# Kernel optimization log

Hardware: AMD Instinct MI355X
Metric: run time of the kernel (lower is better)

The kernel has to match this reference:

```python
import jax, jax.numpy as jnp
import numpy as np

B, N, D_IN, D_OUT = 8, 2048, 1024, 1024


def setup_inputs() -> dict:
    key = jax.random.key(0)
    k0, k1, k2, k3 = jax.random.split(key, 4)
    scale = 1.0 / np.sqrt(D_IN)
    x = jax.random.normal(k0, (B, N, D_IN), dtype=jnp.float32)
    Wq = jax.random.normal(k1, (D_IN, D_OUT), dtype=jnp.float32) * scale
    Wk = jax.random.normal(k2, (D_IN, D_OUT), dtype=jnp.float32) * scale
    Wv = jax.random.normal(k3, (D_IN, D_OUT), dtype=jnp.float32) * scale
    return {"x": x, "Wq": Wq, "Wk": Wk, "Wv": Wv}


def reference(x, Wq, Wk, Wv):
    # x: [b, n, d_in]; single-head causal attention, dropout p=0 (eval).
    q = jnp.einsum('bnd,de->bne', x, Wq)
    k = jnp.einsum('bnd,de->bne', x, Wk)
    v = jnp.einsum('bnd,de->bne', x, Wv)
    n = x.shape[1]
    scores = jnp.einsum('bqe,bke->bqk', q, k)  # [b, n, n]
    causal_mask = jnp.triu(jnp.ones((n, n), dtype=bool), k=1)
    scores = jnp.where(causal_mask, -jnp.inf, scores)
    scale = 1.0 / jnp.sqrt(jnp.asarray(k.shape[-1], dtype=scores.dtype))
    attn = jax.nn.softmax(scores * scale, axis=-1)
    context = jnp.einsum('bqk,bke->bqe', attn, v)
    return context
```

## Files before the change

### kernel.cpp

```cpp
#include <hip/hip_runtime.h>


typedef unsigned short u16;
typedef __bf16 bf16x8 __attribute__((ext_vector_type(8)));
typedef float f32x4 __attribute__((ext_vector_type(4)));
typedef unsigned short u16x8 __attribute__((ext_vector_type(8)));
typedef unsigned short u16x4 __attribute__((ext_vector_type(4)));

static constexpr int BATCH = 8;
static constexpr int SEQ = 2048;
static constexpr int DIM = 1024;

static constexpr size_t SZ_XB = (size_t)BATCH * SEQ * DIM * 2;
static constexpr size_t SZ_W  = (size_t)DIM * DIM * 2;
static constexpr size_t OFF_XB  = 0;
static constexpr size_t OFF_WQT = OFF_XB + SZ_XB;
static constexpr size_t OFF_WKT = OFF_WQT + SZ_W;
static constexpr size_t OFF_WVT = OFF_WKT + SZ_W;
static constexpr size_t OFF_Q   = OFF_WVT + SZ_W;
static constexpr size_t OFF_K   = OFF_Q + SZ_XB;
static constexpr size_t OFF_VT  = OFF_K + SZ_XB;
static constexpr size_t OFF_E   = OFF_VT + SZ_XB;
static constexpr size_t OFF_RS  = OFF_E + (size_t)BATCH * SEQ * SEQ * 2;

__device__ __forceinline__ u16 f2b(float f) {
  unsigned u = __builtin_bit_cast(unsigned, f);
  u += 0x7fffu + ((u >> 16) & 1u);
  return (u16)(u >> 16);
}

__device__ __forceinline__ float b2f(u16 b) {
  return __builtin_bit_cast(float, ((unsigned)b) << 16);
}

__device__ __forceinline__ void gload16(const u16* g, u16* l) {
  __builtin_amdgcn_global_load_lds((__attribute__((address_space(1))) void*)g,
                                   (__attribute__((address_space(3))) void*)l, 16, 0, 0);
}

#define VWAIT(N) asm volatile("s_waitcnt vmcnt(" #N ")" ::: "memory")

__device__ __forceinline__ void barrier_raw() {
  __builtin_amdgcn_sched_barrier(0);
  __builtin_amdgcn_s_barrier();
  __builtin_amdgcn_sched_barrier(0);
}

__global__ __launch_bounds__(256) void cast_f32_bf16(const float* __restrict__ in,
                                                     u16* __restrict__ out) {
  const size_t i = ((size_t)blockIdx.x * 256 + threadIdx.x) * 8;
  float4 a = *(const float4*)(in + i);
  float4 b = *(const float4*)(in + i + 4);
  u16x8 o;
  o[0] = f2b(a.x); o[1] = f2b(a.y); o[2] = f2b(a.z); o[3] = f2b(a.w);
  o[4] = f2b(b.x); o[5] = f2b(b.y); o[6] = f2b(b.z); o[7] = f2b(b.w);
  *reinterpret_cast<u16x8*>(out + i) = o;
}

__global__ __launch_bounds__(256) void transpose_cast_w(const float* __restrict__ W,
                                                        u16* __restrict__ WT) {
  __shared__ float t[32][33];
  const int k0 = blockIdx.x * 32, n0 = blockIdx.y * 32;
  const int tx = threadIdx.x, ty = threadIdx.y;
#pragma unroll
  for (int dy = 0; dy < 32; dy += 8)
    t[ty + dy][tx] = W[(size_t)(k0 + ty + dy) * DIM + n0 + tx];
  __syncthreads();
#pragma unroll
  for (int dy = 0; dy < 32; dy += 8)
    WT[(size_t)(n0 + ty + dy) * DIM + k0 + tx] = f2b(t[tx][ty + dy]);
}

template <int MODE>
__global__ __launch_bounds__(512, 4) void gemm128(
    const u16* __restrict__ A, size_t sA, int lda,
    const u16* __restrict__ Bt, size_t sB, int ldb,
    void* __restrict__ C, size_t sC, int ldc,
    int Kdim, float scale,
    void* __restrict__ C2, void* __restrict__ C3, float* __restrict__ rs) {
  const int bx = blockIdx.x, bz = blockIdx.z;
  int by = (int)blockIdx.y;
  if (MODE == 3) by = (bz < 4) ? (15 - by) : by;
  if (MODE == 2 && 2 * bx > by) return;
  const u16* Ab = A + (size_t)bz * sA;
  const u16* Bb = Bt + (size_t)bz * sB;
  const int rowTile = by * 128, colTile = bx * 256;
  int kmax = Kdim;
  if (MODE == 3) {
    int km = (by + 1) * 128;
    if (km < kmax) kmax = km;
  }
  const int NT = kmax >> 5;

  __shared__ __align__(16) u16 lds[3 * 12288];

  const int tid = threadIdx.x;
  const int w = tid >> 6, l = tid & 63;
  const int wm = w >> 2, wn = w & 3;
  const int lr = l & 15, quad = l >> 4;

  auto srow = [](int c) { int u = (c & 7) ^ ((c >> 3) & 7); return 2 * (c >> 3) + (u >> 2); };
  auto skq  = [](int c) { int u = (c & 7) ^ ((c >> 3) & 7); return u & 3; };
  const u16* pA0 = Ab + (size_t)(rowTile + srow(tid)) * lda + skq(tid) * 8;
  const u16* pB0 = Bb + (size_t)(colTile + srow(tid)) * ldb + skq(tid) * 8;
  const u16* pB1 = Bb + (size_t)(colTile + srow(tid + 512)) * ldb + skq(tid + 512) * 8;

  int offA[4], offB[4];
#pragma unroll
  for (int mi = 0; mi < 4; ++mi) {
    const int row = wm * 64 + mi * 16 + lr;
    offA[mi] = ((row * 64 + quad * 16) ^ (((row >> 1) & 7) << 4)) >> 1;
  }
#pragma unroll
  for (int ni = 0; ni < 4; ++ni) {
    const int row = wn * 64 + ni * 16 + lr;
    offB[ni] = 4096 + ((((row * 64 + quad * 16) ^ (((row >> 1) & 7) << 4))) >> 1);
  }

  f32x4 acc[4][4];
#pragma unroll
  for (int i = 0; i < 4; ++i)
#pragma unroll
    for (int j = 0; j < 4; ++j) acc[i][j] = (f32x4){0.f, 0.f, 0.f, 0.f};

#define STAGE(tt)                                   \
  {                                                 \
    u16* sb = &lds[((unsigned)(tt) % 3u) * 12288];  \
    const int ko = (tt) * 32;                       \
    gload16(pA0 + ko, sb + w * 512);                \
    gload16(pB0 + ko, sb + 4096 + w * 512);         \
    gload16(pB1 + ko, sb + 8192 + w * 512);         \
  }

  STAGE(0);
  STAGE(1);
  VWAIT(3);
  barrier_raw();

  for (int t = 0; t < NT; ++t) {
    const u16* S = &lds[((unsigned)t % 3u) * 12288];
    bf16x8 af[4], bf[4];
#pragma unroll
    for (int mi = 0; mi < 4; ++mi)
      af[mi] = *reinterpret_cast<const bf16x8*>(&S[offA[mi]]);
#pragma unroll
    for (int ni = 0; ni < 4; ++ni)
      bf[ni] = *reinterpret_cast<const bf16x8*>(&S[offB[ni]]);
    if (t + 2 < NT) STAGE(t + 2);
    __builtin_amdgcn_s_setprio(1);
#pragma unroll
    for (int mi = 0; mi < 4; ++mi)
#pragma unroll
      for (int ni = 0; ni < 4; ++ni)
        acc[mi][ni] =
            __builtin_amdgcn_mfma_f32_16x16x32_bf16(af[mi], bf[ni], acc[mi][ni], 0, 0, 0);
    __builtin_amdgcn_s_setprio(0);
    if (t + 2 < NT) {
      VWAIT(3);
    } else if (t + 1 < NT) {
      VWAIT(0);
    }
    asm volatile("s_waitcnt lgkmcnt(0)" ::: "memory");
    barrier_raw();
  }
#undef STAGE

  const int orow0 = rowTile + wm * 64 + quad * 4;
  const int ocol0 = colTile + wn * 64 + lr;

  if (MODE == 4) {
    const int which = colTile >> 10;
    if (which < 2) {
      u16* dst = (which == 0) ? (u16*)C : (u16*)C2;
      const int colL0 = ocol0 & 1023;
#pragma unroll
      for (int mi = 0; mi < 4; ++mi)
#pragma unroll
        for (int ni = 0; ni < 4; ++ni) {
          const int colg = colL0 + ni * 16;
#pragma unroll
          for (int r = 0; r < 4; ++r) {
            const int rowg = orow0 + mi * 16 + r;
            dst[(size_t)rowg * DIM + colg] = f2b(acc[mi][ni][r]);
          }
        }
    } else {
      u16* dst = (u16*)C3;
      const int colL0 = ocol0 & 1023;
#pragma unroll
      for (int mi = 0; mi < 4; ++mi) {
        const int rowg0 = orow0 + mi * 16;
        const int bb = rowg0 >> 11, nn = rowg0 & (SEQ - 1);
#pragma unroll
        for (int ni = 0; ni < 4; ++ni) {
          const int colg = colL0 + ni * 16;
          u16x4 pk;
#pragma unroll
          for (int r = 0; r < 4; ++r) pk[r] = f2b(acc[mi][ni][r]);
          *reinterpret_cast<u16x4*>(
              &dst[(size_t)bb * ((size_t)DIM * SEQ) + (size_t)colg * SEQ + nn]) = pk;
        }
      }
    }
  } else if (MODE == 2) {
#pragma unroll
    for (int mi = 0; mi < 4; ++mi) {
      float rloc[4] = {0.f, 0.f, 0.f, 0.f};
#pragma unroll
      for (int ni = 0; ni < 4; ++ni) {
        const int colg = ocol0 + ni * 16;
#pragma unroll
        for (int r = 0; r < 4; ++r) {
          const int rowg = orow0 + mi * 16 + r;
          const float e = (colg <= rowg) ? __expf(acc[mi][ni][r] * scale) : 0.f;
          const u16 pk = f2b(e);
          ((u16*)C)[(size_t)bz * sC + (size_t)rowg * ldc + colg] = pk;
          rloc[r] += b2f(pk);
        }
      }
#pragma unroll
      for (int r = 0; r < 4; ++r) {
        float v = rloc[r];
        v += __shfl_xor(v, 1);
        v += __shfl_xor(v, 2);
        v += __shfl_xor(v, 4);
        v += __shfl_xor(v, 8);
        if (lr == 0) atomicAdd(&rs[bz * SEQ + orow0 + mi * 16 + r], v);
      }
    }
  } else {
#pragma unroll
    for (int mi = 0; mi < 4; ++mi) {
      float linv[4];
#pragma unroll
      for (int r = 0; r < 4; ++r) linv[r] = 1.f / rs[bz * SEQ + orow0 + mi * 16 + r];
#pragma unroll
      for (int ni = 0; ni < 4; ++ni) {
        const int colg = ocol0 + ni * 16;
#pragma unroll
        for (int r = 0; r < 4; ++r) {
          const int rowg = orow0 + mi * 16 + r;
          ((float*)C)[(size_t)bz * sC + (size_t)rowg * ldc + colg] =
              acc[mi][ni][r] * linv[r];
        }
      }
    }
  }
}

extern "C" void kernel_launch(void* const* d_in, const int* in_sizes, int n_in,
                              void* d_out, int out_size, void* d_ws, size_t ws_size,
                              hipStream_t stream) {
  const float* x = (const float*)d_in[0];
  const float* Wq = (const float*)d_in[1];
  const float* Wk = (const float*)d_in[2];
  const float* Wv = (const float*)d_in[3];
  float* out = (float*)d_out;
  char* ws = (char*)d_ws;

  u16* xb = (u16*)(ws + OFF_XB);
  u16* wqT = (u16*)(ws + OFF_WQT);
  u16* wkT = (u16*)(ws + OFF_WKT);
  u16* wvT = (u16*)(ws + OFF_WVT);
  u16* qb = (u16*)(ws + OFF_Q);
  u16* kb = (u16*)(ws + OFF_K);
  u16* vt = (u16*)(ws + OFF_VT);
  u16* eb = (u16*)(ws + OFF_E);
  float* rsum = (float*)(ws + OFF_RS);

  const int total = BATCH * SEQ * DIM;
  cast_f32_bf16<<<total / (256 * 8), 256, 0, stream>>>(x, xb);
  transpose_cast_w<<<dim3(32, 32), dim3(32, 8), 0, stream>>>(Wq, wqT);
  transpose_cast_w<<<dim3(32, 32), dim3(32, 8), 0, stream>>>(Wk, wkT);
  transpose_cast_w<<<dim3(32, 32), dim3(32, 8), 0, stream>>>(Wv, wvT);
  hipMemsetAsync(rsum, 0, (size_t)BATCH * SEQ * sizeof(float), stream);

  gemm128<4><<<dim3(12, 128, 1), 512, 0, stream>>>(
      xb, 0, DIM, wqT, 0, DIM, qb, 0, DIM, DIM, 1.f, kb, vt, nullptr);
  gemm128<2><<<dim3(8, 16, BATCH), 512, 0, stream>>>(
      qb, (size_t)SEQ * DIM, DIM, kb, (size_t)SEQ * DIM, DIM, eb, (size_t)SEQ * SEQ, SEQ,
      DIM, 0.03125f, nullptr, nullptr, rsum);
  gemm128<3><<<dim3(4, 16, BATCH), 512, 0, stream>>>(
      eb, (size_t)SEQ * SEQ, SEQ, vt, (size_t)DIM * SEQ, SEQ, out, (size_t)SEQ * DIM, DIM,
      SEQ, 1.f, nullptr, nullptr, rsum);
}
```

Measured before the change: 365.4 us.

## Remap GEMM grids to 1D with XCD swizzle, compact causal tiles, pair PV rows

All three GEMMs now use a 1D grid whose block index is remapped with an (o&7)-based swizzle, so that neighbouring tiles land on the same XCD. The QK^T launch enumerates only the causal lower-triangle tiles instead of launching and early-exiting the masked ones. The PV kernel gives each block two row tiles (15-by and by) so every block does the same total K-length of work. The three weight transposes are merged into one launch, and the row-sum memset moves into the projection kernel. This cuts launch overhead, idle blocks and load imbalance, but it relies on the projection kernel having finished zeroing the row sums before the QK^T kernel runs.

Result: no change. 363.0 us (-0.7%).

```diff
diff --git a/kernel.cpp b/kernel.cpp
--- a/kernel.cpp
+++ b/kernel.cpp
@@ -15,9 +15,7 @@
 static constexpr size_t SZ_W  = (size_t)DIM * DIM * 2;
 static constexpr size_t OFF_XB  = 0;
 static constexpr size_t OFF_WQT = OFF_XB + SZ_XB;
-static constexpr size_t OFF_WKT = OFF_WQT + SZ_W;
-static constexpr size_t OFF_WVT = OFF_WKT + SZ_W;
-static constexpr size_t OFF_Q   = OFF_WVT + SZ_W;
+static constexpr size_t OFF_Q   = OFF_WQT + 3 * SZ_W;
 static constexpr size_t OFF_K   = OFF_Q + SZ_XB;
 static constexpr size_t OFF_VT  = OFF_K + SZ_XB;
 static constexpr size_t OFF_E   = OFF_VT + SZ_XB;
@@ -57,9 +55,13 @@
   *reinterpret_cast<u16x8*>(out + i) = o;
 }
 
-__global__ __launch_bounds__(256) void transpose_cast_w(const float* __restrict__ W,
-                                                        u16* __restrict__ WT) {
+__global__ __launch_bounds__(256) void transpose_cast_w3(const float* __restrict__ W0,
+                                                         const float* __restrict__ W1,
+                                                         const float* __restrict__ W2,
+                                                         u16* __restrict__ WT) {
   __shared__ float t[32][33];
+  const float* W = (blockIdx.z == 0) ? W0 : (blockIdx.z == 1) ? W1 : W2;
+  u16* dst = WT + (size_t)blockIdx.z * DIM * DIM;
   const int k0 = blockIdx.x * 32, n0 = blockIdx.y * 32;
   const int tx = threadIdx.x, ty = threadIdx.y;
 #pragma unroll
@@ -68,7 +70,7 @@
   __syncthreads();
 #pragma unroll
   for (int dy = 0; dy < 32; dy += 8)
-    WT[(size_t)(n0 + ty + dy) * DIM + k0 + tx] = f2b(t[tx][ty + dy]);
+    dst[(size_t)(n0 + ty + dy) * DIM + k0 + tx] = f2b(t[tx][ty + dy]);
 }
 
 template <int MODE>
@@ -78,31 +80,48 @@
     void* __restrict__ C, size_t sC, int ldc,
     int Kdim, float scale,
     void* __restrict__ C2, void* __restrict__ C3, float* __restrict__ rs) {
-  const int bx = blockIdx.x, bz = blockIdx.z;
-  int by = (int)blockIdx.y;
-  if (MODE == 3) by = (bz < 4) ? (15 - by) : by;
-  if (MODE == 2 && 2 * bx > by) return;
+  const int tid = threadIdx.x;
+
+  int bx = 0, by = 0, bz = 0, by0 = 0;
+  if (MODE == 4) {
+    if (blockIdx.x == 0) {
+      for (int i = tid; i < BATCH * SEQ; i += 512) rs[i] = 0.f;
+    }
+    const int o = (int)blockIdx.x;
+    const int nw = (o & 7) * 192 + (o >> 3);
+    bx = nw % 12; by = nw / 12;
+  } else if (MODE == 2) {
+    const int o = (int)blockIdx.x;
+    const int nw = (o & 7) * 72 + (o >> 3);
+    bz = nw / 72;
+    int i = nw % 72;
+    int cum = 0;
+#pragma unroll
+    for (int y = 0; y < 16; ++y) {
+      const int c = (y >> 1) + 1;
+      if (i < cum + c) { by = y; bx = i - cum; break; }
+      cum += c;
+    }
+  } else {
+    const int o = (int)blockIdx.x;
+    const int nw = (o & 7) * 32 + (o >> 3);
+    bz = nw >> 5; by0 = (nw >> 2) & 7; bx = nw & 3;
+  }
+
   const u16* Ab = A + (size_t)bz * sA;
   const u16* Bb = Bt + (size_t)bz * sB;
-  const int rowTile = by * 128, colTile = bx * 256;
-  int kmax = Kdim;
-  if (MODE == 3) {
-    int km = (by + 1) * 128;
-    if (km < kmax) kmax = km;
-  }
-  const int NT = kmax >> 5;
+  const int colTile = bx * 256;
 
   __shared__ __align__(16) u16 lds[3 * 12288];
 
-  const int tid = threadIdx.x;
   const int w = tid >> 6, l = tid & 63;
   const int wm = w >> 2, wn = w & 3;
   const int lr = l & 15, quad = l >> 4;
 
   auto srow = [](int c) { int u = (c & 7) ^ ((c >> 3) & 7); return 2 * (c >> 3) + (u >> 2); };
   auto skq  = [](int c) { int u = (c & 7) ^ ((c >> 3) & 7); return u & 3; };
-  const u16* pA0 = Ab + (size_t)(rowTile + srow(tid)) * lda + skq(tid) * 8;
-  const u16* pB0 = Bb + (size_t)(colTile + srow(tid)) * ldb + skq(tid) * 8;
+  const int srA = srow(tid), skA = skq(tid);
+  const u16* pB0 = Bb + (size_t)(colTile + srA) * ldb + skA * 8;
   const u16* pB1 = Bb + (size_t)(colTile + srow(tid + 512)) * ldb + skq(tid + 512) * 8;
 
   int offA[4], offB[4];
@@ -116,12 +135,6 @@
     const int row = wn * 64 + ni * 16 + lr;
     offB[ni] = 4096 + ((((row * 64 + quad * 16) ^ (((row >> 1) & 7) << 4))) >> 1);
   }
-
-  f32x4 acc[4][4];
-#pragma unroll
-  for (int i = 0; i < 4; ++i)
-#pragma unroll
-    for (int j = 0; j < 4; ++j) acc[i][j] = (f32x4){0.f, 0.f, 0.f, 0.f};
 
 #define STAGE(tt)                                   \
   {                                                 \
@@ -132,120 +145,136 @@
     gload16(pB1 + ko, sb + 8192 + w * 512);         \
   }
 
-  STAGE(0);
-  STAGE(1);
-  VWAIT(3);
-  barrier_raw();
-
-  for (int t = 0; t < NT; ++t) {
-    const u16* S = &lds[((unsigned)t % 3u) * 12288];
-    bf16x8 af[4], bf[4];
-#pragma unroll
-    for (int mi = 0; mi < 4; ++mi)
-      af[mi] = *reinterpret_cast<const bf16x8*>(&S[offA[mi]]);
-#pragma unroll
-    for (int ni = 0; ni < 4; ++ni)
-      bf[ni] = *reinterpret_cast<const bf16x8*>(&S[offB[ni]]);
-    if (t + 2 < NT) STAGE(t + 2);
-    __builtin_amdgcn_s_setprio(1);
-#pragma unroll
-    for (int mi = 0; mi < 4; ++mi)
+  const int npass = (MODE == 3) ? 2 : 1;
+  for (int pass = 0; pass < npass; ++pass) {
+    const int byp = (MODE == 3) ? (pass == 0 ? 15 - by0 : by0) : by;
+    const int rowTile = byp * 128;
+    int kmax = Kdim;
+    if (MODE == 3) kmax = (byp + 1) * 128;
+    const int NT = kmax >> 5;
+
+    const u16* pA0 = Ab + (size_t)(rowTile + srA) * lda + skA * 8;
+
+    f32x4 acc[4][4];
+#pragma unroll
+    for (int i = 0; i < 4; ++i)
+#pragma unroll
+      for (int j = 0; j < 4; ++j) acc[i][j] = (f32x4){0.f, 0.f, 0.f, 0.f};
+
+    STAGE(0);
+    STAGE(1);
+    VWAIT(3);
+    barrier_raw();
+
+    for (int t = 0; t < NT; ++t) {
+      const u16* S = &lds[((unsigned)t % 3u) * 12288];
+      bf16x8 af[4], bf[4];
+#pragma unroll
+      for (int mi = 0; mi < 4; ++mi)
+        af[mi] = *reinterpret_cast<const bf16x8*>(&S[offA[mi]]);
 #pragma unroll
       for (int ni = 0; ni < 4; ++ni)
-        acc[mi][ni] =
-            __builtin_amdgcn_mfma_f32_16x16x32_bf16(af[mi], bf[ni], acc[mi][ni], 0, 0, 0);
-    __builtin_amdgcn_s_setprio(0);
-    if (t + 2 < NT) {
-      VWAIT(3);
-    } else if (t + 1 < NT) {
-      VWAIT(0);
+        bf[ni] = *reinterpret_cast<const bf16x8*>(&S[offB[ni]]);
+      if (t + 2 < NT) STAGE(t + 2);
+      __builtin_amdgcn_s_setprio(1);
+#pragma unroll
+      for (int mi = 0; mi < 4; ++mi)
+#pragma unroll
+        for (int ni = 0; ni < 4; ++ni)
+          acc[mi][ni] =
+              __builtin_amdgcn_mfma_f32_16x16x32_bf16(af[mi], bf[ni], acc[mi][ni], 0, 0, 0);
+      __builtin_amdgcn_s_setprio(0);
+      if (t + 2 < NT) {
+        VWAIT(3);
+      } else if (t + 1 < NT) {
+        VWAIT(0);
+      }
+      asm volatile("s_waitcnt lgkmcnt(0)" ::: "memory");
+      barrier_raw();
     }
-    asm volatile("s_waitcnt lgkmcnt(0)" ::: "memory");
-    barrier_raw();
-  }
-#undef STAGE
-
-  const int orow0 = rowTile + wm * 64 + quad * 4;
-  const int ocol0 = colTile + wn * 64 + lr;
-
-  if (MODE == 4) {
-    const int which = colTile >> 10;
-    if (which < 2) {
-      u16* dst = (which == 0) ? (u16*)C : (u16*)C2;
+
+    const int orow0 = rowTile + wm * 64 + quad * 4;
+    const int ocol0 = colTile + wn * 64 + lr;
+
+    if (MODE == 4) {
+      const int which = colTile >> 10;
       const int colL0 = ocol0 & 1023;
-#pragma unroll
-      for (int mi = 0; mi < 4; ++mi)
+      if (which < 2) {
+        u16* dst = (which == 0) ? (u16*)C : (u16*)C2;
+#pragma unroll
+        for (int mi = 0; mi < 4; ++mi)
+#pragma unroll
+          for (int ni = 0; ni < 4; ++ni) {
+            const int colg = colL0 + ni * 16;
+#pragma unroll
+            for (int r = 0; r < 4; ++r) {
+              const int rowg = orow0 + mi * 16 + r;
+              dst[(size_t)rowg * DIM + colg] = f2b(acc[mi][ni][r]);
+            }
+          }
+      } else {
+        u16* dst = (u16*)C3;
+#pragma unroll
+        for (int mi = 0; mi < 4; ++mi) {
+          const int rowg0 = orow0 + mi * 16;
+          const int bb = rowg0 >> 11, nn = rowg0 & (SEQ - 1);
+#pragma unroll
+          for (int ni = 0; ni < 4; ++ni) {
+            const int colg = colL0 + ni * 16;
+            u16x4 pk;
+#pragma unroll
+            for (int r = 0; r < 4; ++r) pk[r] = f2b(acc[mi][ni][r]);
+            *reinterpret_cast<u16x4*>(
+                &dst[(size_t)bb * ((size_t)DIM * SEQ) + (size_t)colg * SEQ + nn]) = pk;
+          }
+        }
+      }
+    } else if (MODE == 2) {
+#pragma unroll
+      for (int mi = 0; mi < 4; ++mi) {
+        float rloc[4] = {0.f, 0.f, 0.f, 0.f};
 #pragma unroll
         for (int ni = 0; ni < 4; ++ni) {
-          const int colg = colL0 + ni * 16;
+          const int colg = ocol0 + ni * 16;
 #pragma unroll
           for (int r = 0; r < 4; ++r) {
             const int rowg = orow0 + mi * 16 + r;
-            dst[(size_t)rowg * DIM + colg] = f2b(acc[mi][ni][r]);
+            const float e = (colg <= rowg) ? __expf(acc[mi][ni][r] * scale) : 0.f;
+            const u16 pk = f2b(e);
+            ((u16*)C)[(size_t)bz * sC + (size_t)rowg * ldc + colg] = pk;
+            rloc[r] += b2f(pk);
           }
         }
+#pragma unroll
+        for (int r = 0; r < 4; ++r) {
+          float v = rloc[r];
+          v += __shfl_xor(v, 1);
+          v += __shfl_xor(v, 2);
+          v += __shfl_xor(v, 4);
+          v += __shfl_xor(v, 8);
+          if (lr == 0) atomicAdd(&rs[bz * SEQ + orow0 + mi * 16 + r], v);
+        }
+      }
     } else {
-      u16* dst = (u16*)C3;
-      const int colL0 = ocol0 & 1023;
 #pragma unroll
       for (int mi = 0; mi < 4; ++mi) {
-        const int rowg0 = orow0 + mi * 16;
-        const int bb = rowg0 >> 11, nn = rowg0 & (SEQ - 1);
+        float linv[4];
+#pragma unroll
+        for (int r = 0; r < 4; ++r) linv[r] = 1.f / rs[bz * SEQ + orow0 + mi * 16 + r];
 #pragma unroll
         for (int ni = 0; ni < 4; ++ni) {
-          const int colg = colL0 + ni * 16;
-          u16x4 pk;
-#pragma unroll
-          for (int r = 0; r < 4; ++r) pk[r] = f2b(acc[mi][ni][r]);
-          *reinterpret_cast<u16x4*>(
-              &dst[(size_t)bb * ((size_t)DIM * SEQ) + (size_t)colg * SEQ + nn]) = pk;
+          const int colg = ocol0 + ni * 16;
+#pragma unroll
+          for (int r = 0; r < 4; ++r) {
+            const int rowg = orow0 + mi * 16 + r;
+            ((float*)C)[(size_t)bz * sC + (size_t)rowg * ldc + colg] =
+                acc[mi][ni][r] * linv[r];
+          }
         }
       }
     }
-  } else if (MODE == 2) {
-#pragma unroll
-    for (int mi = 0; mi < 4; ++mi) {
-      float rloc[4] = {0.f, 0.f, 0.f, 0.f};
-#pragma unroll
-      for (int ni = 0; ni < 4; ++ni) {
-        const int colg = ocol0 + ni * 16;
-#pragma unroll
-        for (int r = 0; r < 4; ++r) {
-          const int rowg = orow0 + mi * 16 + r;
-          const float e = (colg <= rowg) ? __expf(acc[mi][ni][r] * scale) : 0.f;
-          const u16 pk = f2b(e);
-          ((u16*)C)[(size_t)bz * sC + (size_t)rowg * ldc + colg] = pk;
-          rloc[r] += b2f(pk);
-        }
-      }
-#pragma unroll
-      for (int r = 0; r < 4; ++r) {
-        float v = rloc[r];
-        v += __shfl_xor(v, 1);
-        v += __shfl_xor(v, 2);
-        v += __shfl_xor(v, 4);
-        v += __shfl_xor(v, 8);
-        if (lr == 0) atomicAdd(&rs[bz * SEQ + orow0 + mi * 16 + r], v);
-      }
-    }
-  } else {
-#pragma unroll
-    for (int mi = 0; mi < 4; ++mi) {
-      float linv[4];
-#pragma unroll
-      for (int r = 0; r < 4; ++r) linv[r] = 1.f / rs[bz * SEQ + orow0 + mi * 16 + r];
-#pragma unroll
-      for (int ni = 0; ni < 4; ++ni) {
-        const int colg = ocol0 + ni * 16;
-#pragma unroll
-        for (int r = 0; r < 4; ++r) {
-          const int rowg = orow0 + mi * 16 + r;
-          ((float*)C)[(size_t)bz * sC + (size_t)rowg * ldc + colg] =
-              acc[mi][ni][r] * linv[r];
-        }
-      }
-    }
-  }
+  }
+#undef STAGE
 }
 
 extern "C" void kernel_launch(void* const* d_in, const int* in_sizes, int n_in,
@@ -259,9 +288,7 @@
   char* ws = (char*)d_ws;
 
   u16* xb = (u16*)(ws + OFF_XB);
-  u16* wqT = (u16*)(ws + OFF_WQT);
-  u16* wkT = (u16*)(ws + OFF_WKT);
-  u16* wvT = (u16*)(ws + OFF_WVT);
+  u16* wT = (u16*)(ws + OFF_WQT);
   u16* qb = (u16*)(ws + OFF_Q);
   u16* kb = (u16*)(ws + OFF_K);
   u16* vt = (u16*)(ws + OFF_VT);
@@ -270,17 +297,14 @@
 
   const int total = BATCH * SEQ * DIM;
   cast_f32_bf16<<<total / (256 * 8), 256, 0, stream>>>(x, xb);
-  transpose_cast_w<<<dim3(32, 32), dim3(32, 8), 0, stream>>>(Wq, wqT);
-  transpose_cast_w<<<dim3(32, 32), dim3(32, 8), 0, stream>>>(Wk, wkT);
-  transpose_cast_w<<<dim3(32, 32), dim3(32, 8), 0, stream>>>(Wv, wvT);
-  hipMemsetAsync(rsum, 0, (size_t)BATCH * SEQ * sizeof(float), stream);
-
-  gemm128<4><<<dim3(12, 128, 1), 512, 0, stream>>>(
-      xb, 0, DIM, wqT, 0, DIM, qb, 0, DIM, DIM, 1.f, kb, vt, nullptr);
-  gemm128<2><<<dim3(8, 16, BATCH), 512, 0, stream>>>(
+  transpose_cast_w3<<<dim3(32, 32, 3), dim3(32, 8), 0, stream>>>(Wq, Wk, Wv, wT);
+
+  gemm128<4><<<1536, 512, 0, stream>>>(
+      xb, 0, DIM, wT, 0, DIM, qb, 0, DIM, DIM, 1.f, kb, vt, rsum);
+  gemm128<2><<<576, 512, 0, stream>>>(
       qb, (size_t)SEQ * DIM, DIM, kb, (size_t)SEQ * DIM, DIM, eb, (size_t)SEQ * SEQ, SEQ,
       DIM, 0.03125f, nullptr, nullptr, rsum);
-  gemm128<3><<<dim3(4, 16, BATCH), 512, 0, stream>>>(
+  gemm128<3><<<256, 512, 0, stream>>>(
       eb, (size_t)SEQ * SEQ, SEQ, vt, (size_t)DIM * SEQ, SEQ, out, (size_t)SEQ * DIM, DIM,
       SEQ, 1.f, nullptr, nullptr, rsum);
 }
```
